# Kernel tuning notes

Measured on AMD Instinct MI355X. Metric: run time of the kernel, lower is better.

Reference implementation:

```python
import jax, jax.numpy as jnp
import numpy as np

NEG_INF = -9e15
NEG_SLOPE = 0.2

def setup_inputs() -> dict:
    key = jax.random.key(0)
    k1, k2, k3, k4 = jax.random.split(key, 4)
    N, d_in, d_out = 8192, 256, 256
    x = jax.random.normal(k1, (N, d_in), dtype=jnp.float32)
    adj = jax.random.randint(k2, (N, N), 0, 2).astype(jnp.float32)
    W = jax.random.normal(k3, (d_in, d_out), dtype=jnp.float32) * (1.0 / np.sqrt(d_in))
    a = jax.random.normal(k4, (2 * d_out,), dtype=jnp.float32) * (1.0 / np.sqrt(2 * d_out))
    return {"x": x, "adj": adj, "W": W, "a": a}

def reference(x, adj, W, a):
    d_out = W.shape[1]
    Wh = x @ W                                   # [N, d_out]
    # a([Wh_i || Wh_j]) decomposed: e_ij = <a_src, Wh_i> + <a_dst, Wh_j>
    e_src = Wh @ a[:d_out]                       # [N]
    e_dst = Wh @ a[d_out:]                       # [N]
    e = jax.nn.leaky_relu(e_src[:, None] + e_dst[None, :], NEG_SLOPE)  # [N, N]
    N = Wh.shape[0]
    mask = (adj > 0) | jnp.eye(N, dtype=bool)
    e = jnp.where(mask, e, NEG_INF)
    alpha = jax.nn.softmax(e, axis=1)            # [N, N]
    h = alpha @ Wh                               # [N, d_out]
    return h
```

## Files before the change

kernel.cpp:

```cpp
#include <hip/hip_runtime.h>
#include <stdint.h>

#define N 8192
#define D 256

typedef __attribute__((ext_vector_type(4))) float f32x4;
typedef __attribute__((ext_vector_type(8))) short bf16x8;

__device__ __forceinline__ unsigned short f2bf(float f) {
    unsigned u = __float_as_uint(f);
    u += 0x7fff + ((u >> 16) & 1);
    return (unsigned short)(u >> 16);
}
__device__ __forceinline__ float leaky(float x) {
    return fmaxf(x, 0.f) + 0.2f * fminf(x, 0.f);
}
__device__ __forceinline__ void sync_lds() {
    asm volatile("s_waitcnt lgkmcnt(0)\n\ts_barrier" ::: "memory");
}

#define K1_BM 16
__global__ __launch_bounds__(256) void k1_gemm(const float* __restrict__ x,
                                               const float* __restrict__ W,
                                               float* __restrict__ Wh,
                                               unsigned short* __restrict__ WhT) {
    __shared__ float xsT[32][20];
    const int t = threadIdx.x;
    const int r0 = blockIdx.x * K1_BM;
    float acc[K1_BM];
#pragma unroll
    for (int i = 0; i < K1_BM; ++i) acc[i] = 0.f;

    const int lr = t >> 3, lks = (t & 7) * 4;
    float4 xv;
    if (t < 128) xv = *(const float4*)(x + (size_t)(r0 + lr) * D + lks);

    for (int k0 = 0; k0 < D; k0 += 32) {
        __syncthreads();
        if (t < 128) {
            xsT[lks + 0][lr] = xv.x; xsT[lks + 1][lr] = xv.y;
            xsT[lks + 2][lr] = xv.z; xsT[lks + 3][lr] = xv.w;
        }
        __syncthreads();
        if (t < 128 && k0 + 32 < D)
            xv = *(const float4*)(x + (size_t)(r0 + lr) * D + k0 + 32 + lks);
#pragma unroll 8
        for (int kk = 0; kk < 32; ++kk) {
            float wv = W[(size_t)(k0 + kk) * D + t];
#pragma unroll
            for (int rc = 0; rc < K1_BM / 4; ++rc) {
                float4 xr = *(const float4*)&xsT[kk][rc * 4];
                acc[rc * 4 + 0] += xr.x * wv;
                acc[rc * 4 + 1] += xr.y * wv;
                acc[rc * 4 + 2] += xr.z * wv;
                acc[rc * 4 + 3] += xr.w * wv;
            }
        }
    }
#pragma unroll
    for (int r = 0; r < K1_BM; ++r) Wh[(size_t)(r0 + r) * D + t] = acc[r];
    unsigned short pk[K1_BM];
#pragma unroll
    for (int r = 0; r < K1_BM; ++r) pk[r] = f2bf(acc[r]);
    uint4* dst = (uint4*)(WhT + (size_t)t * N + r0);
    dst[0] = *(uint4*)&pk[0];
    dst[1] = *(uint4*)&pk[8];
}

__global__ __launch_bounds__(256) void k2_edot(const float* __restrict__ Wh,
                                               const float* __restrict__ a,
                                               float* __restrict__ e_src,
                                               float* __restrict__ e_dst) {
    const int wave = threadIdx.x >> 6, lane = threadIdx.x & 63;
    const int row = blockIdx.x * 4 + wave;
    float4 wv = *(const float4*)(Wh + (size_t)row * D + lane * 4);
    float4 as = *(const float4*)(a + lane * 4);
    float4 ad = *(const float4*)(a + D + lane * 4);
    float ps = wv.x * as.x + wv.y * as.y + wv.z * as.z + wv.w * as.w;
    float pd = wv.x * ad.x + wv.y * ad.y + wv.z * ad.z + wv.w * ad.w;
#pragma unroll
    for (int m = 1; m < 64; m <<= 1) {
        ps += __shfl_xor(ps, m);
        pd += __shfl_xor(pd, m);
    }
    if (lane == 0) { e_src[row] = ps; e_dst[row] = pd; }
}

__global__ __launch_bounds__(256) void k3_max(const float* __restrict__ e_dst,
                                              float* __restrict__ maxdst) {
    __shared__ float red[4];
    const int t = threadIdx.x;
    float m = -3.4e38f;
    for (int i = t; i < N; i += 256) m = fmaxf(m, e_dst[i]);
#pragma unroll
    for (int msk = 1; msk < 64; msk <<= 1) m = fmaxf(m, __shfl_xor(m, msk));
    if ((t & 63) == 0) red[t >> 6] = m;
    __syncthreads();
    if (t == 0) *maxdst = fmaxf(fmaxf(red[0], red[1]), fmaxf(red[2], red[3]));
}

#define BM 64
#define BK 64
#define RB (N / BM)
#define SPLITS 8
#define NITER ((N / SPLITS) / BK)
#define PSTRIDE 72
__global__ __launch_bounds__(512, 4) void k4_main(const float* __restrict__ adj,
                                                  const unsigned short* __restrict__ WhT,
                                                  const float* __restrict__ e_src,
                                                  const float* __restrict__ e_dst,
                                                  const float* __restrict__ maxdst,
                                                  float* __restrict__ O_part,
                                                  float* __restrict__ l_part) {
    __shared__ unsigned short p_lds[2][BM][PSTRIDE];

    const int t = threadIdx.x;
    const int rb = blockIdx.x >> 3;
    const int s  = blockIdx.x & 7;
    const int r0 = rb * BM;
    const int j0 = s * (N / SPLITS);
    const int rot = ((blockIdx.x >> 8) * 5) & (NITER - 1);

    const int pr = t >> 3;
    const int pc = (t & 7) * 8;
    const int gr = r0 + pr;

    const int w = t >> 6;
    const int lane = t & 63;
    const int quad = lane >> 4, lo = lane & 15;

    const float md = *maxdst;
    const float es = e_src[gr];
    const float m = leaky(es + md);

    f32x4 acc[4][2];
#pragma unroll
    for (int mt = 0; mt < 4; ++mt)
#pragma unroll
        for (int nt = 0; nt < 2; ++nt)
            acc[mt][nt] = (f32x4){0.f, 0.f, 0.f, 0.f};
    float lsum = 0.f;

    const float* adj_row = adj + (size_t)gr * N + j0 + pc;
    const float* ed_row  = e_dst + j0 + pc;
    const unsigned short* wt_base = WhT + (size_t)(w * 32 + lo) * N + j0 + quad * 8;

    auto jtf = [&](int i) {
        int c = (i < NITER) ? i : NITER - 1;
        return (c + rot) & (NITER - 1);
    };

    float4 aA0, aA1;
    float4 aB0, aB1;
    float4 edv0, edv1;
    bf16x8 bfr[2][2];

    auto mma = [&](int cb) {
        __builtin_amdgcn_s_setprio(1);
#pragma unroll
        for (int ks2 = 0; ks2 < 2; ++ks2) {
            bf16x8 afr[4];
#pragma unroll
            for (int mt = 0; mt < 4; ++mt)
                afr[mt] = *(const bf16x8*)&p_lds[cb][mt * 16 + lo][ks2 * 32 + quad * 8];
#pragma unroll
            for (int nt = 0; nt < 2; ++nt)
#pragma unroll
                for (int mt = 0; mt < 4; ++mt)
                    acc[mt][nt] = __builtin_amdgcn_mfma_f32_16x16x32_bf16(
                        afr[mt], bfr[ks2][nt], acc[mt][nt], 0, 0, 0);
        }
        __builtin_amdgcn_s_setprio(0);
    };
    auto bfr_load = [&](int tile) {
#pragma unroll
        for (int ks2 = 0; ks2 < 2; ++ks2)
#pragma unroll
            for (int nt = 0; nt < 2; ++nt)
                bfr[ks2][nt] = *(const bf16x8*)(wt_base + (size_t)nt * (16 * N) +
                                                tile * BK + ks2 * 32);
    };
    auto stage = [&](int tile, int buf, float4 a0, float4 a1, float4 e0, float4 e1) {
        const int jb = j0 + tile * BK + pc;
        float av[8] = {a0.x, a0.y, a0.z, a0.w, a1.x, a1.y, a1.z, a1.w};
        float ev[8] = {e0.x, e0.y, e0.z, e0.w, e1.x, e1.y, e1.z, e1.w};
        unsigned short pk[8];
#pragma unroll
        for (int jj = 0; jj < 8; ++jj) {
            float e = leaky(es + ev[jj]);
            bool keep = (av[jj] > 0.f) || (jb + jj == gr);
            float p = keep ? __expf(e - m) : 0.f;
            lsum += p;
            pk[jj] = f2bf(p);
        }
        *(uint4*)&p_lds[buf][pr][pc] = *(uint4*)pk;
    };

    {
        const int t0 = jtf(0), t1 = jtf(1), t2 = jtf(2);
        aA0 = *(const float4*)(adj_row + t0 * BK);
        aA1 = *(const float4*)(adj_row + t0 * BK + 4);
        aB0 = *(const float4*)(adj_row + t1 * BK);
        aB1 = *(const float4*)(adj_row + t1 * BK + 4);
        edv0 = *(const float4*)(ed_row + t0 * BK);
        edv1 = *(const float4*)(ed_row + t0 * BK + 4);
        bfr_load(t0);
        stage(t0, 0, aA0, aA1, edv0, edv1);
        edv0 = *(const float4*)(ed_row + t1 * BK);
        edv1 = *(const float4*)(ed_row + t1 * BK + 4);
        aA0 = *(const float4*)(adj_row + t2 * BK);
        aA1 = *(const float4*)(adj_row + t2 * BK + 4);
    }
    sync_lds();

    for (int it2 = 0; it2 < NITER / 2; ++it2) {
        {
            const int it = it2 * 2;
            stage(jtf(it + 1), 1, aB0, aB1, edv0, edv1);
            {
                const int tn = jtf(it + 2), tn3 = jtf(it + 3);
                edv0 = *(const float4*)(ed_row + tn * BK);
                edv1 = *(const float4*)(ed_row + tn * BK + 4);
                aB0 = *(const float4*)(adj_row + tn3 * BK);
                aB1 = *(const float4*)(adj_row + tn3 * BK + 4);
            }
            mma(0);
            bfr_load(jtf(it + 1));
            sync_lds();
        }
        {
            const int it = it2 * 2 + 1;
            if (it + 1 < NITER) {
                stage(jtf(it + 1), 0, aA0, aA1, edv0, edv1);
                const int tn = jtf(it + 2), tn3 = jtf(it + 3);
                edv0 = *(const float4*)(ed_row + tn * BK);
                edv1 = *(const float4*)(ed_row + tn * BK + 4);
                aA0 = *(const float4*)(adj_row + tn3 * BK);
                aA1 = *(const float4*)(adj_row + tn3 * BK + 4);
            }
            mma(1);
            bfr_load(jtf(it + 1));
            sync_lds();
        }
    }

#pragma unroll
    for (int msk = 1; msk < 8; msk <<= 1) lsum += __shfl_xor(lsum, msk);
    if ((t & 7) == 0) l_part[(size_t)s * N + gr] = lsum;

#pragma unroll
    for (int mt = 0; mt < 4; ++mt) {
#pragma unroll
        for (int nt = 0; nt < 2; ++nt) {
            f32x4 v = acc[mt][nt];
            int col = w * 32 + nt * 16 + lo;
#pragma unroll
            for (int reg = 0; reg < 4; ++reg) {
                int row = mt * 16 + quad * 4 + reg;
                O_part[((size_t)s * N + r0 + row) * D + col] = v[reg];
            }
        }
    }
}

__global__ __launch_bounds__(256) void k5_reduce(const float* __restrict__ O_part,
                                                 const float* __restrict__ l_part,
                                                 float* __restrict__ out) {
    const int idx = blockIdx.x * 256 + threadIdx.x;
    const int r = idx >> 6;
    float lsum = 0.f;
#pragma unroll
    for (int s = 0; s < SPLITS; ++s) lsum += l_part[(size_t)s * N + r];
    f32x4 o = (f32x4){0.f, 0.f, 0.f, 0.f};
#pragma unroll
    for (int s = 0; s < SPLITS; ++s)
        o += *(const f32x4*)(O_part + (size_t)s * N * D + (size_t)idx * 4);
    const float inv = 1.f / lsum;
    *(f32x4*)(out + (size_t)idx * 4) = o * inv;
}

extern "C" void kernel_launch(void* const* d_in, const int* in_sizes, int n_in,
                              void* d_out, int out_size, void* d_ws, size_t ws_size,
                              hipStream_t stream) {
    const float* x   = (const float*)d_in[0];
    const float* adj = (const float*)d_in[1];
    const float* W   = (const float*)d_in[2];
    const float* a   = (const float*)d_in[3];
    float* out = (float*)d_out;

    char* ws = (char*)d_ws;
    float* Wh            = (float*)(ws);
    unsigned short* WhT  = (unsigned short*)(ws + 8388608);
    float* e_src         = (float*)(ws + 12582912);
    float* e_dst         = (float*)(ws + 12615680);
    float* maxdst        = (float*)(ws + 12648448);
    float* l_part        = (float*)(ws + 12648704);
    float* O_part        = (float*)(ws + 16777216);

    k1_gemm<<<N / K1_BM, 256, 0, stream>>>(x, W, Wh, WhT);
    k2_edot<<<N / 4, 256, 0, stream>>>(Wh, a, e_src, e_dst);
    k3_max<<<1, 256, 0, stream>>>(e_dst, maxdst);
    k4_main<<<RB * SPLITS, 512, 0, stream>>>(adj, WhT, e_src, e_dst, maxdst, O_part, l_part);
    k5_reduce<<<N * D / 4 / 256, 256, 0, stream>>>(O_part, l_part, out);
}
```

Before: 457.1 us.

## Stream adjacency tiles into an LDS ring via direct global-to-LDS loads

Adjacency tiles are now loaded with global_load_lds DMA into a three-slot LDS ring, replacing register-staged prefetching. The e_dst slice is cached in LDS once per block. The row tile is halved to 32 rows so occupancy can rise to 8 blocks per CU. The goal is to hide adjacency load latency and cut register pressure, but each WhT fragment is now reused over fewer rows, which roughly doubles WhT traffic. The manual vmcnt accounting is also fragile.

```diff
diff --git a/kernel.cpp b/kernel.cpp
--- a/kernel.cpp
+++ b/kernel.cpp
@@ -15,9 +15,11 @@
 __device__ __forceinline__ float leaky(float x) {
     return fmaxf(x, 0.f) + 0.2f * fminf(x, 0.f);
 }
-__device__ __forceinline__ void sync_lds() {
-    asm volatile("s_waitcnt lgkmcnt(0)\n\ts_barrier" ::: "memory");
-}
+
+#define GLOAD_LDS(gsrc, lptr)                                                          \
+    __builtin_amdgcn_global_load_lds(                                                  \
+        (const __attribute__((address_space(1))) unsigned int*)(gsrc),                 \
+        (__attribute__((address_space(3))) unsigned int*)(lptr), 16, 0, 0)
 
 #define K1_BM 16
 __global__ __launch_bounds__(256) void k1_gemm(const float* __restrict__ x,
@@ -99,13 +101,14 @@
     if (t == 0) *maxdst = fmaxf(fmaxf(red[0], red[1]), fmaxf(red[2], red[3]));
 }
 
-#define BM 64
+#define BM 32
 #define BK 64
 #define RB (N / BM)
 #define SPLITS 8
 #define NITER ((N / SPLITS) / BK)
 #define PSTRIDE 72
-__global__ __launch_bounds__(512, 4) void k4_main(const float* __restrict__ adj,
+#define RING 3
+__global__ __launch_bounds__(512, 8) void k4_main(const float* __restrict__ adj,
                                                   const unsigned short* __restrict__ WhT,
                                                   const float* __restrict__ e_src,
                                                   const float* __restrict__ e_dst,
@@ -113,6 +116,8 @@
                                                   float* __restrict__ O_part,
                                                   float* __restrict__ l_part) {
     __shared__ unsigned short p_lds[2][BM][PSTRIDE];
+    __shared__ float adj_ring[RING][BM][BK];
+    __shared__ float ed_lds[N / SPLITS];
 
     const int t = threadIdx.x;
     const int rb = blockIdx.x >> 3;
@@ -121,8 +126,8 @@
     const int j0 = s * (N / SPLITS);
     const int rot = ((blockIdx.x >> 8) * 5) & (NITER - 1);
 
-    const int pr = t >> 3;
-    const int pc = (t & 7) * 8;
+    const int pr = t >> 4;
+    const int pc4 = (t & 15) * 4;
     const int gr = r0 + pr;
 
     const int w = t >> 6;
@@ -133,16 +138,14 @@
     const float es = e_src[gr];
     const float m = leaky(es + md);
 
-    f32x4 acc[4][2];
-#pragma unroll
-    for (int mt = 0; mt < 4; ++mt)
+    f32x4 acc[2][2];
+#pragma unroll
+    for (int mt = 0; mt < 2; ++mt)
 #pragma unroll
         for (int nt = 0; nt < 2; ++nt)
             acc[mt][nt] = (f32x4){0.f, 0.f, 0.f, 0.f};
     float lsum = 0.f;
 
-    const float* adj_row = adj + (size_t)gr * N + j0 + pc;
-    const float* ed_row  = e_dst + j0 + pc;
     const unsigned short* wt_base = WhT + (size_t)(w * 32 + lo) * N + j0 + quad * 8;
 
     auto jtf = [&](int i) {
@@ -150,23 +153,20 @@
         return (c + rot) & (NITER - 1);
     };
 
-    float4 aA0, aA1;
-    float4 aB0, aB1;
-    float4 edv0, edv1;
     bf16x8 bfr[2][2];
 
     auto mma = [&](int cb) {
         __builtin_amdgcn_s_setprio(1);
 #pragma unroll
         for (int ks2 = 0; ks2 < 2; ++ks2) {
-            bf16x8 afr[4];
-#pragma unroll
-            for (int mt = 0; mt < 4; ++mt)
+            bf16x8 afr[2];
+#pragma unroll
+            for (int mt = 0; mt < 2; ++mt)
                 afr[mt] = *(const bf16x8*)&p_lds[cb][mt * 16 + lo][ks2 * 32 + quad * 8];
 #pragma unroll
             for (int nt = 0; nt < 2; ++nt)
 #pragma unroll
-                for (int mt = 0; mt < 4; ++mt)
+                for (int mt = 0; mt < 2; ++mt)
                     acc[mt][nt] = __builtin_amdgcn_mfma_f32_16x16x32_bf16(
                         afr[mt], bfr[ks2][nt], acc[mt][nt], 0, 0, 0);
         }
@@ -180,76 +180,64 @@
                 bfr[ks2][nt] = *(const bf16x8*)(wt_base + (size_t)nt * (16 * N) +
                                                 tile * BK + ks2 * 32);
     };
-    auto stage = [&](int tile, int buf, float4 a0, float4 a1, float4 e0, float4 e1) {
-        const int jb = j0 + tile * BK + pc;
-        float av[8] = {a0.x, a0.y, a0.z, a0.w, a1.x, a1.y, a1.z, a1.w};
-        float ev[8] = {e0.x, e0.y, e0.z, e0.w, e1.x, e1.y, e1.z, e1.w};
-        unsigned short pk[8];
-#pragma unroll
-        for (int jj = 0; jj < 8; ++jj) {
+    auto dma = [&](int tile, int slot) {
+        const float* src = adj + (size_t)gr * N + j0 + tile * BK + pc4;
+        GLOAD_LDS(src, &adj_ring[slot][pr][pc4]);
+    };
+    auto stage_ring = [&](int tile, int buf, int slot) {
+        const int jb = j0 + tile * BK + pc4;
+        f32x4 av = *(const f32x4*)&adj_ring[slot][pr][pc4];
+        f32x4 ev = *(const f32x4*)&ed_lds[tile * BK + pc4];
+        unsigned short pk[4];
+#pragma unroll
+        for (int jj = 0; jj < 4; ++jj) {
             float e = leaky(es + ev[jj]);
             bool keep = (av[jj] > 0.f) || (jb + jj == gr);
             float p = keep ? __expf(e - m) : 0.f;
             lsum += p;
             pk[jj] = f2bf(p);
         }
-        *(uint4*)&p_lds[buf][pr][pc] = *(uint4*)pk;
+        *(uint2*)&p_lds[buf][pr][pc4] = *(uint2*)pk;
     };
 
     {
-        const int t0 = jtf(0), t1 = jtf(1), t2 = jtf(2);
-        aA0 = *(const float4*)(adj_row + t0 * BK);
-        aA1 = *(const float4*)(adj_row + t0 * BK + 4);
-        aB0 = *(const float4*)(adj_row + t1 * BK);
-        aB1 = *(const float4*)(adj_row + t1 * BK + 4);
-        edv0 = *(const float4*)(ed_row + t0 * BK);
-        edv1 = *(const float4*)(ed_row + t0 * BK + 4);
+        ed_lds[t] = e_dst[j0 + t];
+        ed_lds[512 + t] = e_dst[j0 + 512 + t];
+        const int t0 = jtf(0);
+        const int jb = j0 + t0 * BK + pc4;
+        f32x4 av = *(const f32x4*)(adj + (size_t)gr * N + jb);
+        f32x4 ev = *(const f32x4*)(e_dst + jb);
         bfr_load(t0);
-        stage(t0, 0, aA0, aA1, edv0, edv1);
-        edv0 = *(const float4*)(ed_row + t1 * BK);
-        edv1 = *(const float4*)(ed_row + t1 * BK + 4);
-        aA0 = *(const float4*)(adj_row + t2 * BK);
-        aA1 = *(const float4*)(adj_row + t2 * BK + 4);
-    }
-    sync_lds();
-
-    for (int it2 = 0; it2 < NITER / 2; ++it2) {
-        {
-            const int it = it2 * 2;
-            stage(jtf(it + 1), 1, aB0, aB1, edv0, edv1);
-            {
-                const int tn = jtf(it + 2), tn3 = jtf(it + 3);
-                edv0 = *(const float4*)(ed_row + tn * BK);
-                edv1 = *(const float4*)(ed_row + tn * BK + 4);
-                aB0 = *(const float4*)(adj_row + tn3 * BK);
-                aB1 = *(const float4*)(adj_row + tn3 * BK + 4);
-            }
-            mma(0);
-            bfr_load(jtf(it + 1));
-            sync_lds();
-        }
-        {
-            const int it = it2 * 2 + 1;
-            if (it + 1 < NITER) {
-                stage(jtf(it + 1), 0, aA0, aA1, edv0, edv1);
-                const int tn = jtf(it + 2), tn3 = jtf(it + 3);
-                edv0 = *(const float4*)(ed_row + tn * BK);
-                edv1 = *(const float4*)(ed_row + tn * BK + 4);
-                aA0 = *(const float4*)(adj_row + tn3 * BK);
-                aA1 = *(const float4*)(adj_row + tn3 * BK + 4);
-            }
-            mma(1);
-            bfr_load(jtf(it + 1));
-            sync_lds();
-        }
-    }
-
-#pragma unroll
-    for (int msk = 1; msk < 8; msk <<= 1) lsum += __shfl_xor(lsum, msk);
-    if ((t & 7) == 0) l_part[(size_t)s * N + gr] = lsum;
-
-#pragma unroll
-    for (int mt = 0; mt < 4; ++mt) {
+        unsigned short pk[4];
+#pragma unroll
+        for (int jj = 0; jj < 4; ++jj) {
+            float e = leaky(es + ev[jj]);
+            bool keep = (av[jj] > 0.f) || (jb + jj == gr);
+            float p = keep ? __expf(e - m) : 0.f;
+            lsum += p;
+            pk[jj] = f2bf(p);
+        }
+        *(uint2*)&p_lds[0][pr][pc4] = *(uint2*)pk;
+        dma(jtf(1), 1 % RING);
+        dma(jtf(2), 2 % RING);
+    }
+    asm volatile("s_waitcnt vmcnt(0) lgkmcnt(0)\n\ts_barrier" ::: "memory");
+
+#pragma unroll 2
+    for (int it = 0; it < NITER; ++it) {
+        if (it + 1 < NITER) stage_ring(jtf(it + 1), (it + 1) & 1, (it + 1) % RING);
+        mma(it & 1);
+        if (it + 1 < NITER) bfr_load(jtf(it + 1));
+        if (it + 3 < NITER) dma(jtf(it + 3), (it + 3) % RING);
+        asm volatile("s_waitcnt vmcnt(4) lgkmcnt(0)\n\ts_barrier" ::: "memory");
+    }
+
+#pragma unroll
+    for (int msk = 1; msk < 16; msk <<= 1) lsum += __shfl_xor(lsum, msk);
+    if ((t & 15) == 0) l_part[(size_t)s * N + gr] = lsum;
+
+#pragma unroll
+    for (int mt = 0; mt < 2; ++mt) {
 #pragma unroll
         for (int nt = 0; nt < 2; ++nt) {
             f32x4 v = acc[mt][nt];
```

Measured after the change: 491.5 us. +7.5%, slower.

## Drop softmax max pass, use raw exp2 with prescaled logits and packed bf16 convert

Applied to the files above, without the earlier changes.

Folds log2(e) into e_src/e_dst so the main kernel can use the hardware v_exp_f32 directly. It removes the max-subtraction and with it the separate single-block max-reduction kernel and its launch. The per-element diagonal check is replaced by a precomputed per-thread test applied once. Two floats are packed to bf16 per instruction instead of rounding manually. Without max subtraction, large logits could overflow; that relies on the value range of these inputs.

```diff
diff --git a/kernel.cpp b/kernel.cpp
--- a/kernel.cpp
+++ b/kernel.cpp
@@ -3,6 +3,7 @@
 
 #define N 8192
 #define D 256
+#define LOG2E 1.44269504f
 
 typedef __attribute__((ext_vector_type(4))) float f32x4;
 typedef __attribute__((ext_vector_type(8))) short bf16x8;
@@ -14,6 +15,11 @@
 }
 __device__ __forceinline__ float leaky(float x) {
     return fmaxf(x, 0.f) + 0.2f * fminf(x, 0.f);
+}
+__device__ __forceinline__ float exp2_raw(float x) {
+    float r;
+    asm("v_exp_f32 %0, %1" : "=v"(r) : "v"(x));
+    return r;
 }
 __device__ __forceinline__ void sync_lds() {
     asm volatile("s_waitcnt lgkmcnt(0)\n\ts_barrier" ::: "memory");
@@ -83,20 +89,7 @@
         ps += __shfl_xor(ps, m);
         pd += __shfl_xor(pd, m);
     }
-    if (lane == 0) { e_src[row] = ps; e_dst[row] = pd; }
-}
-
-__global__ __launch_bounds__(256) void k3_max(const float* __restrict__ e_dst,
-                                              float* __restrict__ maxdst) {
-    __shared__ float red[4];
-    const int t = threadIdx.x;
-    float m = -3.4e38f;
-    for (int i = t; i < N; i += 256) m = fmaxf(m, e_dst[i]);
-#pragma unroll
-    for (int msk = 1; msk < 64; msk <<= 1) m = fmaxf(m, __shfl_xor(m, msk));
-    if ((t & 63) == 0) red[t >> 6] = m;
-    __syncthreads();
-    if (t == 0) *maxdst = fmaxf(fmaxf(red[0], red[1]), fmaxf(red[2], red[3]));
+    if (lane == 0) { e_src[row] = ps * LOG2E; e_dst[row] = pd * LOG2E; }
 }
 
 #define BM 64
@@ -109,7 +102,6 @@
                                                   const unsigned short* __restrict__ WhT,
                                                   const float* __restrict__ e_src,
                                                   const float* __restrict__ e_dst,
-                                                  const float* __restrict__ maxdst,
                                                   float* __restrict__ O_part,
                                                   float* __restrict__ l_part) {
     __shared__ unsigned short p_lds[2][BM][PSTRIDE];
@@ -129,9 +121,12 @@
     const int lane = t & 63;
     const int quad = lane >> 4, lo = lane & 15;
 
-    const float md = *maxdst;
     const float es = e_src[gr];
-    const float m = leaky(es + md);
+
+    const int dcol = gr - j0;
+    const int dtile = dcol >> 6;
+    const int djj = dcol & 7;
+    const bool hd = ((unsigned)dcol < (unsigned)(N / SPLITS)) && ((dcol & 56) == pc);
 
     f32x4 acc[4][2];
 #pragma unroll
@@ -181,19 +176,24 @@
                                                 tile * BK + ks2 * 32);
     };
     auto stage = [&](int tile, int buf, float4 a0, float4 a1, float4 e0, float4 e1) {
-        const int jb = j0 + tile * BK + pc;
         float av[8] = {a0.x, a0.y, a0.z, a0.w, a1.x, a1.y, a1.z, a1.w};
         float ev[8] = {e0.x, e0.y, e0.z, e0.w, e1.x, e1.y, e1.z, e1.w};
-        unsigned short pk[8];
+        float pv[8];
 #pragma unroll
         for (int jj = 0; jj < 8; ++jj) {
-            float e = leaky(es + ev[jj]);
-            bool keep = (av[jj] > 0.f) || (jb + jj == gr);
-            float p = keep ? __expf(e - m) : 0.f;
-            lsum += p;
-            pk[jj] = f2bf(p);
-        }
-        *(uint4*)&p_lds[buf][pr][pc] = *(uint4*)pk;
+            float p = exp2_raw(leaky(es + ev[jj]));
+            pv[jj] = (av[jj] > 0.f) ? p : 0.f;
+        }
+        if (hd && tile == dtile)
+            pv[djj] = exp2_raw(leaky(es + ev[djj]));
+#pragma unroll
+        for (int jj = 0; jj < 8; ++jj) lsum += pv[jj];
+        unsigned wpk[4];
+#pragma unroll
+        for (int jj = 0; jj < 4; ++jj)
+            asm("v_cvt_pk_bf16_f32 %0, %1, %2"
+                : "=v"(wpk[jj]) : "v"(pv[2 * jj]), "v"(pv[2 * jj + 1]));
+        *(uint4*)&p_lds[buf][pr][pc] = *(uint4*)wpk;
     };
 
     {
@@ -293,13 +293,11 @@
     unsigned short* WhT  = (unsigned short*)(ws + 8388608);
     float* e_src         = (float*)(ws + 12582912);
     float* e_dst         = (float*)(ws + 12615680);
-    float* maxdst        = (float*)(ws + 12648448);
     float* l_part        = (float*)(ws + 12648704);
     float* O_part        = (float*)(ws + 16777216);
 
     k1_gemm<<<N / K1_BM, 256, 0, stream>>>(x, W, Wh, WhT);
     k2_edot<<<N / 4, 256, 0, stream>>>(Wh, a, e_src, e_dst);
-    k3_max<<<1, 256, 0, stream>>>(e_dst, maxdst);
-    k4_main<<<RB * SPLITS, 512, 0, stream>>>(adj, WhT, e_src, e_dst, maxdst, O_part, l_part);
+    k4_main<<<RB * SPLITS, 512, 0, stream>>>(adj, WhT, e_src, e_dst, O_part, l_part);
     k5_reduce<<<N * D / 4 / 256, 256, 0, stream>>>(O_part, l_part, out);
 }
```

Result: faster. 445.4 us (-2.6%).
